# Optimization experiments

Hardware: AMD Instinct MI355X
Metric: run time of the kernel (lower is better)

The kernel has to match this reference:

```python
import jax, jax.numpy as jnp
import numpy as np

LL_SIGMA = 1.0   # ll_sigma
P_SIGMA = 1.0    # p_sigma
RBF_SIGMA = 1.0  # rbf_sigma
STEP_SIZE = 0.1  # step_svgd default step_size

N_PART, HID, DIN, BATCH = 64, 1024, 16, 2048
PARAM_SCALE = 0.01  # keeps pairwise RBF kernel non-degenerate (||ti-tj||^2 ~ O(1))


def setup_inputs() -> dict:
    key = jax.random.key(0)
    ks = jax.random.split(key, 6)
    W1 = jax.random.normal(ks[0], (N_PART, HID, DIN), dtype=jnp.float32) * PARAM_SCALE
    b1 = jax.random.normal(ks[1], (N_PART, HID), dtype=jnp.float32) * PARAM_SCALE
    W2 = jax.random.normal(ks[2], (N_PART, 1, HID), dtype=jnp.float32) * PARAM_SCALE
    b2 = jax.random.normal(ks[3], (N_PART, 1), dtype=jnp.float32) * PARAM_SCALE
    X = jax.random.normal(ks[4], (BATCH, DIN), dtype=jnp.float32)
    y = jax.random.normal(ks[5], (BATCH,), dtype=jnp.float32)
    return {"W1": W1, "b1": b1, "W2": W2, "b2": b2, "X": X, "y": y}


def _flatten(W1, b1, W2, b2):
    # Flatten each particle's params into one row -> [N, D], D = HID*DIN + HID + HID + 1
    n = W1.shape[0]
    return jnp.concatenate(
        [W1.reshape(n, -1), b1.reshape(n, -1), W2.reshape(n, -1), b2.reshape(n, -1)],
        axis=1,
    )


def _log_posterior(w1, bb1, w2, bb2, X, y):
    # Particle MLP forward: Linear -> relu -> Linear (scalar output), Gaussian LL + Gaussian prior
    h = jax.nn.relu(X @ w1.T + bb1)            # [B, HID]
    yhat = (h @ w2.T + bb2)[:, 0]              # [B]
    ll = -0.5 * jnp.sum((y - yhat) ** 2) / (LL_SIGMA ** 2)
    lp = -0.5 * (jnp.sum(w1 ** 2) + jnp.sum(bb1 ** 2)
                 + jnp.sum(w2 ** 2) + jnp.sum(bb2 ** 2)) / (P_SIGMA ** 2)
    return ll + lp


def reference(W1, b1, W2, b2, X, y):
    """One fused step_svgd: returns updated flattened particles [N, D].

    kd[i,j] = exp(-||ti - tj||^2 / (2 rbf^2))
    dkd[i][j] (grad of kd(zi,zj) wrt zj, as stored by step_svgd) = kd[i,j]*(ti - tj)/rbf^2
    theta_i += step/N * sum_j ( kd[i,j] * dlogpost[j] + dkd[i][j] )
    """
    n = W1.shape[0]
    theta = _flatten(W1, b1, W2, b2)                       # [N, D]

    # Pairwise RBF kernel (stable squared-distance form)
    sq = jnp.sum(theta ** 2, axis=1)                       # [N]
    d2 = jnp.maximum(sq[:, None] + sq[None, :] - 2.0 * theta @ theta.T, 0.0)
    kd = jnp.exp(-d2 / (2.0 * RBF_SIGMA ** 2))             # [N, N]

    # Per-particle log-posterior gradients (vmapped autodiff)
    grads = jax.vmap(jax.grad(_log_posterior, argnums=(0, 1, 2, 3)),
                     in_axes=(0, 0, 0, 0, None, None))(W1, b1, W2, b2, X, y)
    dlog = _flatten(*grads)                                # [N, D]

    # sum_j kd[i,j]*(ti - tj)/rbf^2 computed without the [N,N,D] tensor
    s = jnp.sum(kd, axis=1)                                # [N]
    kernel_grad = (theta * s[:, None] - kd @ theta) / (RBF_SIGMA ** 2)
    phi = kd @ dlog + kernel_grad                          # [N, D]

    return theta + (STEP_SIZE / n) * phi
```

## Files before the change

### kernel.cpp

```cpp
#include <hip/hip_runtime.h>

#define NP 64
#define HID 1024
#define DIN 16
#define BATCH 2048
#define DTOT 18433
#define OFF_B1 16384
#define OFF_W2 17408
#define OFF_B2 18432
#define STEPC 0.0015625f
#define GCH 128
#define NGBLK 145

typedef __attribute__((ext_vector_type(8))) short bf16x8;
typedef __attribute__((ext_vector_type(4))) short short4v;
typedef __attribute__((ext_vector_type(4))) float f32x4;

__device__ __forceinline__ short f2bf(float f) {
  union { float f; unsigned u; } v; v.f = f;
  unsigned r = v.u + 0x7FFFu + ((v.u >> 16) & 1u);
  return (short)(r >> 16);
}

__device__ __forceinline__ float theta_at(int i, int d,
    const float* __restrict__ W1, const float* __restrict__ b1,
    const float* __restrict__ W2, const float* __restrict__ b2) {
  if (d < OFF_B1) return W1[i * 16384 + d];
  if (d < OFF_W2) return b1[i * HID + (d - OFF_B1)];
  if (d < OFF_B2) return W2[i * HID + (d - OFF_W2)];
  return b2[i];
}

__global__ __launch_bounds__(256) void k_prep(
    const float* __restrict__ W1, const float* __restrict__ X,
    short* __restrict__ W1b, short* __restrict__ Xb, short* __restrict__ XtS) {
  const int gid = blockIdx.x * 256 + threadIdx.x;
  {
    const size_t base = (size_t)gid * 8;
    f32x4 a = *(const f32x4*)&W1[base];
    f32x4 b = *(const f32x4*)&W1[base + 4];
    bf16x8 o;
    o[0] = f2bf(a[0]); o[1] = f2bf(a[1]); o[2] = f2bf(a[2]); o[3] = f2bf(a[3]);
    o[4] = f2bf(b[0]); o[5] = f2bf(b[1]); o[6] = f2bf(b[2]); o[7] = f2bf(b[3]);
    *(bf16x8*)&W1b[base] = o;
  }
  if (gid < 4096) {
    const size_t base = (size_t)gid * 8;
    f32x4 a = *(const f32x4*)&X[base];
    f32x4 b = *(const f32x4*)&X[base + 4];
    bf16x8 o;
    o[0] = f2bf(a[0]); o[1] = f2bf(a[1]); o[2] = f2bf(a[2]); o[3] = f2bf(a[3]);
    o[4] = f2bf(b[0]); o[5] = f2bf(b[1]); o[6] = f2bf(b[2]); o[7] = f2bf(b[3]);
    *(bf16x8*)&Xb[base] = o;
  }
  if (gid < 2048) {
    const int d = gid & 15;
    const int b0 = (gid >> 4) * 16;
    #pragma unroll
    for (int q = 0; q < 4; ++q) {
      short4v s4;
      #pragma unroll
      for (int t = 0; t < 4; ++t) s4[t] = f2bf(X[(b0 + q * 4 + t) * DIN + d]);
      *(short4v*)&XtS[d * 2048 + b0 + q * 4] = s4;
    }
  }
}

__global__ __launch_bounds__(512) void k_fwd_gram(
    const short* __restrict__ W1b, const float* __restrict__ b1,
    const float* __restrict__ W2, const float* __restrict__ b2,
    const short* __restrict__ Xb, const float* __restrict__ y,
    short* __restrict__ ebf_ws, float* __restrict__ Pb2,
    const float* __restrict__ W1, float* __restrict__ gpart) {
  __shared__ __align__(16) char smem[34816];
  const int bx = blockIdx.x;
  const int tid = threadIdx.x;

  if (bx < 512) {
    const int n = bx >> 3, bg = bx & 7;
    const int w = tid >> 6, l = tid & 63;
    const int lrow = l & 15, lhi = l >> 4;
    float (*yhp)[256] = (float (*)[256])smem;
    float* pbl = (float*)(smem + 8192);

    const bf16x8 zf = {0, 0, 0, 0, 0, 0, 0, 0};
    bf16x8 af[8];
    f32x4 b1v[8], w2v[8];
    #pragma unroll
    for (int ktl = 0; ktl < 8; ++ktl) {
      const int krow = n * HID + (w * 8 + ktl) * 16;
      af[ktl] = (lhi < 2) ? *(const bf16x8*)&W1b[(size_t)(krow + lrow) * DIN + lhi * 8] : zf;
      b1v[ktl] = *(const f32x4*)&b1[krow + lhi * 4];
      w2v[ktl] = *(const f32x4*)&W2[krow + lhi * 4];
    }

    for (int bt = 0; bt < 16; ++bt) {
      const int bbase = bg * 256 + bt * 16;
      const bf16x8 bf = (lhi < 2) ? *(const bf16x8*)&Xb[(size_t)(bbase + lrow) * DIN + lhi * 8] : zf;
      float ya = 0.f;
      #pragma unroll
      for (int ktl = 0; ktl < 8; ++ktl) {
        f32x4 c = {0.f, 0.f, 0.f, 0.f};
        c = __builtin_amdgcn_mfma_f32_16x16x32_bf16(af[ktl], bf, c, 0, 0, 0);
        #pragma unroll
        for (int r = 0; r < 4; ++r) {
          const float pre = c[r] + b1v[ktl][r];
          ya = fmaf(fmaxf(pre, 0.f), w2v[ktl][r], ya);
        }
      }
      ya += __shfl_xor(ya, 16);
      ya += __shfl_xor(ya, 32);
      if (l < 16) yhp[w][bt * 16 + lrow] = ya;
    }
    __syncthreads();
    float ev = 0.f;
    if (tid < 256) {
      float sum = 0.f;
      #pragma unroll
      for (int q = 0; q < 8; ++q) sum += yhp[q][tid];
      const int b = bg * 256 + tid;
      ev = y[b] - (sum + b2[n]);
      ebf_ws[n * BATCH + b] = f2bf(ev);
    }
    #pragma unroll
    for (int off = 1; off < 64; off <<= 1) ev += __shfl_xor(ev, off);
    if (tid < 256 && l == 0) pbl[w] = ev;
    __syncthreads();
    if (tid == 0) Pb2[n * 8 + bg] = pbl[0] + pbl[1] + pbl[2] + pbl[3];
  } else {
    float (*ths)[68] = (float (*)[68])smem;
    const int gb = bx - 512;
    const int c0 = gb * GCH;
    for (int idx = tid; idx < 2048; idx += 512) {
      const int i = idx >> 5;
      const int dd = (idx & 31) * 4;
      const int d = c0 + dd;
      float v0, v1, v2, v3;
      if (d + 3 < DTOT) {
        f32x4 q;
        if (d < OFF_B1)      q = *(const f32x4*)&W1[i * 16384 + d];
        else if (d < OFF_W2) q = *(const f32x4*)&b1[i * HID + (d - OFF_B1)];
        else                 q = *(const f32x4*)&W2[i * HID + (d - OFF_W2)];
        v0 = q[0]; v1 = q[1]; v2 = q[2]; v3 = q[3];
      } else {
        v0 = (d     < DTOT) ? theta_at(i, d,     W1, b1, W2, b2) : 0.f;
        v1 = (d + 1 < DTOT) ? theta_at(i, d + 1, W1, b1, W2, b2) : 0.f;
        v2 = (d + 2 < DTOT) ? theta_at(i, d + 2, W1, b1, W2, b2) : 0.f;
        v3 = (d + 3 < DTOT) ? theta_at(i, d + 3, W1, b1, W2, b2) : 0.f;
      }
      ths[dd][i] = v0; ths[dd + 1][i] = v1; ths[dd + 2][i] = v2; ths[dd + 3][i] = v3;
    }
    __syncthreads();
    if (tid < 256) {
      const int i0 = (tid >> 4) << 2;
      const int j0 = (tid & 15) << 2;
      float acc[4][4] = {};
      for (int dc = 0; dc < 128; ++dc) {
        const f32x4 av = *(const f32x4*)&ths[dc][i0];
        const f32x4 bv = *(const f32x4*)&ths[dc][j0];
        #pragma unroll
        for (int a = 0; a < 4; ++a)
          #pragma unroll
          for (int bj = 0; bj < 4; ++bj)
            acc[a][bj] = fmaf(av[a], bv[bj], acc[a][bj]);
      }
      float* __restrict__ gp = gpart + gb * 4096;
      #pragma unroll
      for (int a = 0; a < 4; ++a)
        #pragma unroll
        for (int bj = 0; bj < 4; ++bj)
          gp[(i0 + a) * 64 + j0 + bj] = acc[a][bj];
    }
  }
}

__global__ __launch_bounds__(512) void k_bwd_red(
    const float* __restrict__ b1, const short* __restrict__ W1b,
    const short* __restrict__ Xb, const short* __restrict__ XtS,
    const short* __restrict__ ebf_ws, float* __restrict__ dwp,
    float* __restrict__ gbp, const float* __restrict__ gpart,
    float* __restrict__ gram) {
  __shared__ __align__(16) char smem[34816];
  const int bx = blockIdx.x;
  const int tid = threadIdx.x;

  if (bx < 1024) {
    const int n = bx >> 4, kg = (bx >> 1) & 7, bs = bx & 1;
    const int w = tid >> 6, l = tid & 63;
    const int lrow = l & 15, lhi = l >> 4;
    short* __restrict__ Xa  = (short*)smem;
    short* __restrict__ Xt  = (short*)(smem + 8192);
    short* __restrict__ Gt  = (short*)(smem + 16384);
    short* __restrict__ els = (short*)(smem + 32768);

    if (tid < 256)
      *(short4v*)&els[tid * 4] = *(const short4v*)&ebf_ws[n * BATCH + bs * 1024 + tid * 4];

    const int kt_g = kg * 8 + w;
    const int kglob = kt_g * 16 + lrow;
    const bf16x8 zf = {0, 0, 0, 0, 0, 0, 0, 0};
    const short one_bf = (short)0x3F80;
    const bf16x8 onesf = {one_bf, one_bf, one_bf, one_bf, one_bf, one_bf, one_bf, one_bf};
    const bf16x8 b1f = (lhi < 2) ? *(const bf16x8*)&W1b[(size_t)(n * HID + kglob) * DIN + lhi * 8] : zf;
    const float b1r = b1[n * HID + kglob];
    short* __restrict__ GtW = &Gt[w * 1024];
    const int xw = (lrow & 7) << 3;
    f32x4 c2 = {0.f, 0.f, 0.f, 0.f};
    f32x4 c3 = {0.f, 0.f, 0.f, 0.f};

    auto computeG = [&](int ch, int bt8, short* __restrict__ slot) {
      #pragma unroll
      for (int rt = 0; rt < 2; ++rt) {
        const int bl = bt8 * 32 + rt * 16 + lrow;
        const bf16x8 a1 = (lhi < 2) ? *(const bf16x8*)&Xa[(bl * 16 + lhi * 8) ^ xw] : zf;
        f32x4 c1 = {0.f, 0.f, 0.f, 0.f};
        c1 = __builtin_amdgcn_mfma_f32_16x16x32_bf16(a1, b1f, c1, 0, 0, 0);
        const short4v es = *(const short4v*)&els[ch * 256 + bt8 * 32 + rt * 16 + lhi * 4];
        short4v gg;
        #pragma unroll
        for (int r = 0; r < 4; ++r) {
          const float pre = c1[r] + b1r;
          gg[r] = (pre > 0.f) ? es[r] : (short)0;
        }
        *(short4v*)&slot[(lrow * 32 + rt * 16 + lhi * 4) ^ xw] = gg;
      }
    };

    for (int ch = 0; ch < 4; ++ch) {
      __syncthreads();
      {
        const int b = tid >> 1, half = tid & 1;
        *(bf16x8*)&Xa[(b * 16 + half * 8) ^ ((b & 7) << 3)] =
            *(const bf16x8*)&Xb[(size_t)(bs * 1024 + ch * 256 + b) * DIN + half * 8];
        const int d = tid >> 5, c8 = (tid & 31) * 8;
        *(bf16x8*)&Xt[(d * 256 + c8) ^ ((d & 7) << 3)] =
            *(const bf16x8*)&XtS[d * 2048 + bs * 1024 + ch * 256 + c8];
      }
      __syncthreads();
      computeG(ch, 0, GtW);
      #pragma unroll
      for (int bt8 = 0; bt8 < 8; ++bt8) {
        short* __restrict__ cur = &GtW[(bt8 & 1) * 512];
        short* __restrict__ nxt = &GtW[((bt8 & 1) ^ 1) * 512];
        const bf16x8 a2f = *(const bf16x8*)&cur[(lrow * 32 + lhi * 8) ^ xw];
        const bf16x8 b2f = *(const bf16x8*)&Xt[(lrow * 256 + bt8 * 32 + lhi * 8) ^ xw];
        if (bt8 < 7) computeG(ch, bt8 + 1, nxt);
        c2 = __builtin_amdgcn_mfma_f32_16x16x32_bf16(a2f, b2f, c2, 0, 0, 0);
        c3 = __builtin_amdgcn_mfma_f32_16x16x32_bf16(a2f, onesf, c3, 0, 0, 0);
      }
    }

    float* __restrict__ dw = dwp + (size_t)(bs * NP + n) * HID * 16;
    #pragma unroll
    for (int r = 0; r < 4; ++r)
      dw[(kt_g * 16 + lhi * 4 + r) * 16 + lrow] = c2[r];
    const int l3 = l & 3;
    const float gv = (l3 == 0) ? c3[0] : (l3 == 1) ? c3[1] : (l3 == 2) ? c3[2] : c3[3];
    const int src = (((l & 15) >> 2) << 4) | (l & 15);
    const float gb1v = __shfl(gv, src);
    if (l < 16)
      gbp[(size_t)(bs * NP + n) * HID + kt_g * 16 + l] = gb1v;
  } else {
    float (*red)[64] = (float (*)[64])smem;
    const int gb = bx - 1024;
    const int pl = tid & 63;
    const int sl = tid >> 6;
    const int pair = gb * 64 + pl;
    float a = 0.f;
    for (int p = sl; p < NGBLK; p += 8) a += gpart[p * 4096 + pair];
    red[sl][pl] = a;
    __syncthreads();
    if (tid < 64) {
      float t = 0.f;
      #pragma unroll
      for (int q = 0; q < 8; ++q) t += red[q][tid];
      gram[gb * 64 + tid] = t;
    }
  }
}

__global__ __launch_bounds__(128) void k_fin(
    const float* __restrict__ W1, const float* __restrict__ b1,
    const float* __restrict__ W2, const float* __restrict__ b2,
    const float* __restrict__ dwp, const float* __restrict__ gbp,
    const float* __restrict__ Pb2, float* __restrict__ vout) {
  const int n = blockIdx.x, kg = blockIdx.y;
  const int k = kg * 128 + threadIdx.x;
  const size_t nk = (size_t)n * HID + k;
  const f32x4* p0 = (const f32x4*)&dwp[nk * 16];
  const f32x4* p1 = (const f32x4*)&dwp[(nk + (size_t)NP * HID) * 16];
  const f32x4* wrow = (const f32x4*)&W1[nk * 16];
  const float w2r = W2[nk], b1r = b1[nk];
  const float gb1 = gbp[nk] + gbp[nk + (size_t)NP * HID];
  float dot = 0.f;
  float* __restrict__ vr = vout + (size_t)n * DTOT + (size_t)k * 16;
  #pragma unroll
  for (int q = 0; q < 4; ++q) {
    const f32x4 s = p0[q] + p1[q];
    const f32x4 ww = wrow[q];
    #pragma unroll
    for (int c = 0; c < 4; ++c) {
      vr[q * 4 + c] = s[c] * w2r - 2.f * ww[c];
      dot = fmaf(s[c], ww[c], dot);
    }
  }
  vout[(size_t)n * DTOT + OFF_B1 + k] = gb1 * w2r - 2.f * b1r;
  vout[(size_t)n * DTOT + OFF_W2 + k] = (dot + b1r * gb1) - 2.f * w2r;
  if (kg == 0 && threadIdx.x == 0) {
    float sb = 0.f;
    #pragma unroll
    for (int q = 0; q < 8; ++q) sb += Pb2[n * 8 + q];
    vout[(size_t)n * DTOT + OFF_B2] = sb - 2.f * b2[n];
  }
}

__global__ __launch_bounds__(256) void k_update(
    const float* __restrict__ W1, const float* __restrict__ b1,
    const float* __restrict__ W2, const float* __restrict__ b2,
    const float* __restrict__ gram, float* __restrict__ vout) {
  __shared__ float Vs[64][132];
  __shared__ float kds[4096];
  __shared__ float ss[64];
  __shared__ float sq[64];
  const int c0 = blockIdx.x * GCH;
  const int cols = min(GCH, DTOT - c0);
  for (int idx = threadIdx.x; idx < 64 * GCH; idx += 256) {
    const int i = idx >> 7, dd = idx & 127;
    Vs[i][dd] = (dd < cols) ? vout[(size_t)i * DTOT + c0 + dd] : 0.f;
  }
  if (threadIdx.x < 64) sq[threadIdx.x] = gram[threadIdx.x * 65];
  __syncthreads();
  for (int q = threadIdx.x; q < 4096; q += 256) {
    const int i = q >> 6, j = q & 63;
    const float d2 = fmaxf(sq[i] + sq[j] - 2.f * gram[q], 0.f);
    kds[q] = expf(-0.5f * d2);
  }
  __syncthreads();
  if (threadIdx.x < 64) {
    float a = 0.f;
    for (int j = 0; j < 64; ++j) a += kds[threadIdx.x * 64 + j];
    ss[threadIdx.x] = a;
  }
  __syncthreads();
  const int col4 = (threadIdx.x & 31) * 4;
  const int i0 = (threadIdx.x >> 5) * 8;
  f32x4 acc[8] = {};
  for (int j = 0; j < 64; ++j) {
    const f32x4 vv = *(const f32x4*)&Vs[j][col4];
    const f32x4 k0 = *(const f32x4*)&kds[j * 64 + i0];
    const f32x4 k1 = *(const f32x4*)&kds[j * 64 + i0 + 4];
    #pragma unroll
    for (int a = 0; a < 4; ++a) {
      acc[a][0] = fmaf(k0[a], vv[0], acc[a][0]);
      acc[a][1] = fmaf(k0[a], vv[1], acc[a][1]);
      acc[a][2] = fmaf(k0[a], vv[2], acc[a][2]);
      acc[a][3] = fmaf(k0[a], vv[3], acc[a][3]);
    }
    #pragma unroll
    for (int a = 0; a < 4; ++a) {
      acc[a + 4][0] = fmaf(k1[a], vv[0], acc[a + 4][0]);
      acc[a + 4][1] = fmaf(k1[a], vv[1], acc[a + 4][1]);
      acc[a + 4][2] = fmaf(k1[a], vv[2], acc[a + 4][2]);
      acc[a + 4][3] = fmaf(k1[a], vv[3], acc[a + 4][3]);
    }
  }
  #pragma unroll
  for (int a = 0; a < 8; ++a) {
    const int i = i0 + a;
    const float f = 1.f + STEPC * ss[i];
    #pragma unroll
    for (int cc = 0; cc < 4; ++cc) {
      const int d = c0 + col4 + cc;
      if (d < DTOT) {
        const float th = theta_at(i, d, W1, b1, W2, b2);
        vout[(size_t)i * DTOT + d] = th * f + STEPC * acc[a][cc];
      }
    }
  }
}

extern "C" void kernel_launch(void* const* d_in, const int* in_sizes, int n_in,
                              void* d_out, int out_size, void* d_ws, size_t ws_size,
                              hipStream_t stream) {
  const float* W1 = (const float*)d_in[0];
  const float* b1 = (const float*)d_in[1];
  const float* W2 = (const float*)d_in[2];
  const float* b2 = (const float*)d_in[3];
  const float* X  = (const float*)d_in[4];
  const float* y  = (const float*)d_in[5];
  float* vout = (float*)d_out;

  float* Pb2   = (float*)d_ws;
  float* gpart = Pb2 + 512;
  float* gram  = gpart + NGBLK * 4096;
  float* dwp   = gram + 4096;
  float* gbp   = dwp + 2 * NP * HID * 16;
  short* W1b   = (short*)(gbp + 2 * NP * HID);
  short* Xb    = W1b + NP * HID * DIN;
  short* XtS   = Xb + BATCH * DIN;
  short* ebf   = XtS + BATCH * DIN;

  k_prep<<<512, 256, 0, stream>>>(W1, X, W1b, Xb, XtS);
  k_fwd_gram<<<512 + NGBLK, 512, 0, stream>>>(W1b, b1, W2, b2, Xb, y, ebf, Pb2, W1, gpart);
  k_bwd_red<<<1024 + 64, 512, 0, stream>>>(b1, W1b, Xb, XtS, ebf, dwp, gbp, gpart, gram);
  k_fin<<<dim3(NP, 8), 128, 0, stream>>>(W1, b1, W2, b2, dwp, gbp, Pb2, vout);
  k_update<<<NGBLK, 256, 0, stream>>>(W1, b1, W2, b2, gram, vout);
}
```

Before: 92.79 us.

## Fuse gradient finalization into SVGD update kernel, removing intermediate V round-trip

Removes the separate k_fin kernel and computes the per-particle combined gradient/prior vector directly into shared memory inside k_update, branching on which parameter segment the column block covers. This eliminates one kernel launch and a full write-then-read of the N x D intermediate in global memory. The W2 segment now does 16-wide strided dot products per element inside fewer blocks, which may create load imbalance.

```diff
diff --git a/kernel.cpp b/kernel.cpp
--- a/kernel.cpp
+++ b/kernel.cpp
@@ -279,71 +279,95 @@
   }
 }
 
-__global__ __launch_bounds__(128) void k_fin(
-    const float* __restrict__ W1, const float* __restrict__ b1,
-    const float* __restrict__ W2, const float* __restrict__ b2,
-    const float* __restrict__ dwp, const float* __restrict__ gbp,
-    const float* __restrict__ Pb2, float* __restrict__ vout) {
-  const int n = blockIdx.x, kg = blockIdx.y;
-  const int k = kg * 128 + threadIdx.x;
-  const size_t nk = (size_t)n * HID + k;
-  const f32x4* p0 = (const f32x4*)&dwp[nk * 16];
-  const f32x4* p1 = (const f32x4*)&dwp[(nk + (size_t)NP * HID) * 16];
-  const f32x4* wrow = (const f32x4*)&W1[nk * 16];
-  const float w2r = W2[nk], b1r = b1[nk];
-  const float gb1 = gbp[nk] + gbp[nk + (size_t)NP * HID];
-  float dot = 0.f;
-  float* __restrict__ vr = vout + (size_t)n * DTOT + (size_t)k * 16;
-  #pragma unroll
-  for (int q = 0; q < 4; ++q) {
-    const f32x4 s = p0[q] + p1[q];
-    const f32x4 ww = wrow[q];
-    #pragma unroll
-    for (int c = 0; c < 4; ++c) {
-      vr[q * 4 + c] = s[c] * w2r - 2.f * ww[c];
-      dot = fmaf(s[c], ww[c], dot);
-    }
-  }
-  vout[(size_t)n * DTOT + OFF_B1 + k] = gb1 * w2r - 2.f * b1r;
-  vout[(size_t)n * DTOT + OFF_W2 + k] = (dot + b1r * gb1) - 2.f * w2r;
-  if (kg == 0 && threadIdx.x == 0) {
-    float sb = 0.f;
-    #pragma unroll
-    for (int q = 0; q < 8; ++q) sb += Pb2[n * 8 + q];
-    vout[(size_t)n * DTOT + OFF_B2] = sb - 2.f * b2[n];
-  }
-}
-
 __global__ __launch_bounds__(256) void k_update(
     const float* __restrict__ W1, const float* __restrict__ b1,
     const float* __restrict__ W2, const float* __restrict__ b2,
-    const float* __restrict__ gram, float* __restrict__ vout) {
+    const float* __restrict__ gram, const float* __restrict__ dwp,
+    const float* __restrict__ gbp, const float* __restrict__ Pb2,
+    float* __restrict__ vout) {
   __shared__ float Vs[64][132];
   __shared__ float kds[4096];
   __shared__ float ss[64];
   __shared__ float sq[64];
   const int c0 = blockIdx.x * GCH;
-  const int cols = min(GCH, DTOT - c0);
-  for (int idx = threadIdx.x; idx < 64 * GCH; idx += 256) {
-    const int i = idx >> 7, dd = idx & 127;
-    Vs[i][dd] = (dd < cols) ? vout[(size_t)i * DTOT + c0 + dd] : 0.f;
-  }
-  if (threadIdx.x < 64) sq[threadIdx.x] = gram[threadIdx.x * 65];
+  const int tid = threadIdx.x;
+
+  if (c0 + GCH <= OFF_B1) {
+    for (int idx = tid; idx < 2048; idx += 256) {
+      const int i = idx >> 5, dd = (idx & 31) * 4;
+      const size_t o = (size_t)i * 16384 + c0 + dd;
+      const f32x4 s0 = *(const f32x4*)&dwp[o];
+      const f32x4 s1 = *(const f32x4*)&dwp[o + (size_t)NP * 16384];
+      const f32x4 ww = *(const f32x4*)&W1[o];
+      const float w2r = W2[i * HID + ((c0 + dd) >> 4)];
+      #pragma unroll
+      for (int c = 0; c < 4; ++c)
+        Vs[i][dd + c] = (s0[c] + s1[c]) * w2r - 2.f * ww[c];
+    }
+  } else if (c0 + GCH <= OFF_W2) {
+    for (int idx = tid; idx < 2048; idx += 256) {
+      const int i = idx >> 5, dd = (idx & 31) * 4;
+      const size_t o = (size_t)i * HID + (c0 + dd - OFF_B1);
+      const f32x4 g0 = *(const f32x4*)&gbp[o];
+      const f32x4 g1 = *(const f32x4*)&gbp[o + (size_t)NP * HID];
+      const f32x4 w2v = *(const f32x4*)&W2[o];
+      const f32x4 b1v = *(const f32x4*)&b1[o];
+      #pragma unroll
+      for (int c = 0; c < 4; ++c)
+        Vs[i][dd + c] = (g0[c] + g1[c]) * w2v[c] - 2.f * b1v[c];
+    }
+  } else if (c0 + GCH <= OFF_B2) {
+    for (int idx = tid; idx < 2048; idx += 256) {
+      const int i = idx >> 5, dd = (idx & 31) * 4;
+      #pragma unroll
+      for (int c = 0; c < 4; ++c) {
+        const int k = c0 + dd + c - OFF_W2;
+        const size_t nk = (size_t)i * HID + k;
+        const f32x4* p0 = (const f32x4*)&dwp[nk * 16];
+        const f32x4* p1 = (const f32x4*)&dwp[(nk + (size_t)NP * HID) * 16];
+        const f32x4* wr = (const f32x4*)&W1[nk * 16];
+        float dot = 0.f;
+        #pragma unroll
+        for (int q = 0; q < 4; ++q) {
+          const f32x4 s = p0[q] + p1[q];
+          const f32x4 ww = wr[q];
+          dot = fmaf(s[0], ww[0], dot); dot = fmaf(s[1], ww[1], dot);
+          dot = fmaf(s[2], ww[2], dot); dot = fmaf(s[3], ww[3], dot);
+        }
+        const float gb1 = gbp[nk] + gbp[nk + (size_t)NP * HID];
+        Vs[i][dd + c] = (dot + b1[nk] * gb1) - 2.f * W2[nk];
+      }
+    }
+  } else {
+    for (int idx = tid; idx < 2048; idx += 256) {
+      const int i = idx >> 5, dd = (idx & 31) * 4;
+      f32x4 v = {0.f, 0.f, 0.f, 0.f};
+      if (dd == 0) {
+        float sb = 0.f;
+        #pragma unroll
+        for (int q = 0; q < 8; ++q) sb += Pb2[i * 8 + q];
+        v[0] = sb - 2.f * b2[i];
+      }
+      *(f32x4*)&Vs[i][dd] = v;
+    }
+  }
+
+  if (tid < 64) sq[tid] = gram[tid * 65];
   __syncthreads();
-  for (int q = threadIdx.x; q < 4096; q += 256) {
+  for (int q = tid; q < 4096; q += 256) {
     const int i = q >> 6, j = q & 63;
     const float d2 = fmaxf(sq[i] + sq[j] - 2.f * gram[q], 0.f);
     kds[q] = expf(-0.5f * d2);
   }
   __syncthreads();
-  if (threadIdx.x < 64) {
+  if (tid < 64) {
     float a = 0.f;
-    for (int j = 0; j < 64; ++j) a += kds[threadIdx.x * 64 + j];
-    ss[threadIdx.x] = a;
+    for (int j = 0; j < 64; ++j) a += kds[tid * 64 + j];
+    ss[tid] = a;
   }
   __syncthreads();
-  const int col4 = (threadIdx.x & 31) * 4;
-  const int i0 = (threadIdx.x >> 5) * 8;
+  const int col4 = (tid & 31) * 4;
+  const int i0 = (tid >> 5) * 8;
   f32x4 acc[8] = {};
   for (int j = 0; j < 64; ++j) {
     const f32x4 vv = *(const f32x4*)&Vs[j][col4];
@@ -403,6 +427,5 @@
   k_prep<<<512, 256, 0, stream>>>(W1, X, W1b, Xb, XtS);
   k_fwd_gram<<<512 + NGBLK, 512, 0, stream>>>(W1b, b1, W2, b2, Xb, y, ebf, Pb2, W1, gpart);
   k_bwd_red<<<1024 + 64, 512, 0, stream>>>(b1, W1b, Xb, XtS, ebf, dwp, gbp, gpart, gram);
-  k_fin<<<dim3(NP, 8), 128, 0, stream>>>(W1, b1, W2, b2, dwp, gbp, Pb2, vout);
-  k_update<<<NGBLK, 256, 0, stream>>>(W1, b1, W2, b2, gram, vout);
-}
+  k_update<<<NGBLK, 256, 0, stream>>>(W1, b1, W2, b2, gram, dwp, gbp, Pb2, vout);
+}
```

Measured after the change: 124.1 us. +33.7%, slower.
